# Optimization experiments

Measured on AMD Instinct MI355X. Metric: run time of the kernel, lower is better.

The kernel has to match this reference:

```python
import jax, jax.numpy as jnp
import numpy as np

DIM = 256
HEADS = 4
DIM_HEAD = 32
HIDDEN = HEADS * DIM_HEAD  # 128
SCALE = DIM_HEAD ** -0.5
EPS = 1e-5


def setup_inputs() -> dict:
    key = jax.random.key(0)
    ks = jax.random.split(key, 6)
    b, h, w = 4, 64, 64
    x = jax.random.normal(ks[0], (b, DIM, h, w), dtype=jnp.float32)
    # GroupNorm(1, dim) affine params
    gamma = jnp.ones((DIM,), dtype=jnp.float32)
    beta = jnp.zeros((DIM,), dtype=jnp.float32)
    # 1x1 convs as dense matrices over channels
    w_qkv = jax.random.normal(ks[1], (3 * HIDDEN, DIM), dtype=jnp.float32) * (DIM ** -0.5)
    w_out = jax.random.normal(ks[2], (DIM, HIDDEN), dtype=jnp.float32) * (HIDDEN ** -0.5)
    b_out = jax.random.normal(ks[3], (DIM,), dtype=jnp.float32) * 0.02
    return {"x": x, "gamma": gamma, "beta": beta, "w_qkv": w_qkv,
            "w_out": w_out, "b_out": b_out}


def reference(x, gamma, beta, w_qkv, w_out, b_out):
    b, c, h, w = x.shape
    n = h * w
    # GroupNorm with 1 group == layernorm over (C,H,W) per sample, per-channel affine
    mu = jnp.mean(x, axis=(1, 2, 3), keepdims=True)
    var = jnp.var(x, axis=(1, 2, 3), keepdims=True)
    xn = (x - mu) * jax.lax.rsqrt(var + EPS)
    xn = xn * gamma[None, :, None, None] + beta[None, :, None, None]
    # 1x1 conv -> qkv, then split into heads; flatten spatial dims to n = h*w
    qkv = jnp.einsum('bchw,oc->bohw', xn, w_qkv)            # (b, 3*hidden, h, w)
    qkv = qkv.reshape(b, 3, HEADS, DIM_HEAD, n)
    q, k, v = qkv[:, 0], qkv[:, 1], qkv[:, 2]               # (b, heads, dim_head, n)
    q = q * SCALE
    sim = jnp.einsum('bhci,bhcj->bhij', q, k)               # (b, heads, n, n)
    attn = jax.nn.softmax(sim, axis=-1)                     # stable softmax (max subtract)
    out = jnp.einsum('bhij,bhcj->bhic', attn, v)            # (b, heads, n, dim_head)
    out = out.transpose(0, 1, 3, 2).reshape(b, HIDDEN, h, w)
    y = jnp.einsum('bchw,oc->bohw', out, w_out) + b_out[None, :, None, None]
    return y
```

## Files before the change

kernel.cpp:

```cpp
#include <hip/hip_runtime.h>
#include <math.h>

#define BATCH 4
#define CDIM 256
#define NPIX 4096
#define NPB (CDIM * NPIX)
#define HEADS 4
#define DH 32
#define HID 128
#define OQKV 384
#define QK_SCALE (0.1767766952966369f * 1.44269504088896340736f)
#define SOFTMAX_C 10.0f
#define LN_EPS 1e-5f

typedef _Float16 f16;
typedef _Float16 f16x8 __attribute__((ext_vector_type(8)));
typedef _Float16 f16x4 __attribute__((ext_vector_type(4)));
typedef float f32x4 __attribute__((ext_vector_type(4)));

__device__ __forceinline__ void gload16(const void* g, void* l) {
  __builtin_amdgcn_global_load_lds(
      (const __attribute__((address_space(1))) void*)g,
      (__attribute__((address_space(3))) void*)l, 16, 0, 0);
}

union U8u { unsigned int u[4]; f16x8 v; };
union U8h { f16 h[8]; f16x8 v; };

__global__ __launch_bounds__(256) void ln_reduce(const float* __restrict__ x,
                                                 float* __restrict__ part) {
  const int blk = blockIdx.x;
  const int b = blk >> 6;
  const int slice = blk & 63;
  const float4* xp = (const float4*)(x + (size_t)b * NPB) + (size_t)slice * 4096;
  const int t = threadIdx.x;
  float s = 0.f, ss = 0.f;
#pragma unroll
  for (int k = 0; k < 16; ++k) {
    float4 v = xp[t + k * 256];
    s += v.x + v.y + v.z + v.w;
    ss += v.x * v.x + v.y * v.y + v.z * v.z + v.w * v.w;
  }
#pragma unroll
  for (int d = 1; d < 64; d <<= 1) {
    s += __shfl_xor(s, d);
    ss += __shfl_xor(ss, d);
  }
  __shared__ float red[8];
  const int wv = t >> 6;
  if ((t & 63) == 0) { red[wv * 2] = s; red[wv * 2 + 1] = ss; }
  __syncthreads();
  if (t == 0) {
    part[blk * 2]     = red[0] + red[2] + red[4] + red[6];
    part[blk * 2 + 1] = red[1] + red[3] + red[5] + red[7];
  }
}

__global__ void ln_finalize(const float* __restrict__ part, float* __restrict__ stats) {
  const int t = threadIdx.x;
  const int b = t >> 6, lane = t & 63;
  float s  = part[(b * 64 + lane) * 2];
  float ss = part[(b * 64 + lane) * 2 + 1];
#pragma unroll
  for (int d = 1; d < 64; d <<= 1) {
    s += __shfl_xor(s, d);
    ss += __shfl_xor(ss, d);
  }
  if (lane == 0) {
    float mu = s * (1.f / (float)NPB);
    float var = ss * (1.f / (float)NPB) - mu * mu;
    stats[b * 2] = mu;
    stats[b * 2 + 1] = rsqrtf(var + LN_EPS);
  }
}

__global__ __launch_bounds__(256) void qkv_gemm(const float* __restrict__ x,
                                                const float* __restrict__ gamma,
                                                const float* __restrict__ beta,
                                                const float* __restrict__ wqkv,
                                                const float* __restrict__ stats,
                                                f16* __restrict__ qT,
                                                f16* __restrict__ kT,
                                                f16* __restrict__ vO) {
  const int b = blockIdx.z;
  const int oclass = blockIdx.y;
  const int p0 = blockIdx.x * 128;
  const int t = threadIdx.x;
  const int w = t >> 6, lane = t & 63, low4 = lane & 15, quad = lane >> 4;
  const int ow0 = (w >> 1) * 64, pw0 = (w & 1) * 64;
  const float mu = stats[2 * b], rstd = stats[2 * b + 1];
  const float wscale = (oclass == 0) ? QK_SCALE : 1.f;

  __shared__ f16 Ws[128 * 40];
  __shared__ float Xs[32 * 132];

  const int wo = t >> 1, wh = (t & 1) * 16;
  const int xc = t >> 3, xpq = (t & 7) * 16;
  const float* wg = wqkv + (size_t)(oclass * 128 + wo) * CDIM + wh;
  const float* xg = x + ((size_t)b * CDIM + xc) * NPIX + p0 + xpq;

  f32x4 acc[4][4] = {};
  f32x4 wr[4], xr[4];
  {
    const float ga = gamma[xc] * rstd;
    const float bb = beta[xc] - mu * ga;
#pragma unroll
    for (int j = 0; j < 4; ++j) {
      wr[j] = *(const f32x4*)(wg + j * 4);
      f32x4 r = *(const f32x4*)(xg + j * 4);
      r[0] = r[0] * ga + bb; r[1] = r[1] * ga + bb;
      r[2] = r[2] * ga + bb; r[3] = r[3] * ga + bb;
      xr[j] = r;
    }
  }

  for (int ks = 0; ks < 8; ++ks) {
    __syncthreads();
    {
      U8h h0, h1;
#pragma unroll
      for (int e = 0; e < 4; ++e) {
        h0.h[e]     = (f16)(wr[0][e] * wscale);
        h0.h[4 + e] = (f16)(wr[1][e] * wscale);
        h1.h[e]     = (f16)(wr[2][e] * wscale);
        h1.h[4 + e] = (f16)(wr[3][e] * wscale);
      }
      *(f16x8*)&Ws[wo * 40 + wh]     = h0.v;
      *(f16x8*)&Ws[wo * 40 + wh + 8] = h1.v;
#pragma unroll
      for (int j = 0; j < 4; ++j)
        *(f32x4*)&Xs[xc * 132 + xpq + 4 * j] = xr[j];
    }
    __syncthreads();

    if (ks < 7) {
      const int k0n = (ks + 1) * 32;
      const float ga = gamma[k0n + xc] * rstd;
      const float bb = beta[k0n + xc] - mu * ga;
#pragma unroll
      for (int j = 0; j < 4; ++j) {
        wr[j] = *(const f32x4*)(wg + k0n + j * 4);
        f32x4 r = *(const f32x4*)(xg + (size_t)k0n * NPIX + j * 4);
        r[0] = r[0] * ga + bb; r[1] = r[1] * ga + bb;
        r[2] = r[2] * ga + bb; r[3] = r[3] * ga + bb;
        xr[j] = r;
      }
    }

    f16x8 wf[4], xf[4];
#pragma unroll
    for (int i = 0; i < 4; ++i)
      wf[i] = *(const f16x8*)&Ws[(ow0 + i * 16 + low4) * 40 + quad * 8];
#pragma unroll
    for (int j = 0; j < 4; ++j) {
      const int pl = pw0 + j * 16 + low4;
      U8u xv;
#pragma unroll
      for (int r = 0; r < 4; ++r) {
        const float e0 = Xs[(quad * 8 + 2 * r) * 132 + pl];
        const float e1 = Xs[(quad * 8 + 2 * r + 1) * 132 + pl];
        xv.u[r] = __builtin_bit_cast(unsigned int,
                    __builtin_amdgcn_cvt_pkrtz(e0, e1));
      }
      xf[j] = xv.v;
    }

    if (oclass < 2) {
#pragma unroll
      for (int i = 0; i < 4; ++i)
#pragma unroll
        for (int j = 0; j < 4; ++j)
          acc[i][j] = __builtin_amdgcn_mfma_f32_16x16x32_f16(wf[i], xf[j], acc[i][j], 0, 0, 0);
    } else {
#pragma unroll
      for (int i = 0; i < 4; ++i)
#pragma unroll
        for (int j = 0; j < 4; ++j)
          acc[i][j] = __builtin_amdgcn_mfma_f32_16x16x32_f16(xf[i], wf[j], acc[i][j], 0, 0, 0);
    }
  }

  if (oclass < 2) {
    f16* dst = (oclass == 0) ? qT : kT;
#pragma unroll
    for (int i = 0; i < 4; ++i) {
      const int o_loc = ow0 + i * 16 + quad * 4;
      const int hh = o_loc >> 5;
      const int cb = o_loc & 31;
      f16* base = dst + ((size_t)(b * HEADS + hh) * NPIX) * DH + cb;
#pragma unroll
      for (int j = 0; j < 4; ++j) {
        const int p = p0 + pw0 + j * 16 + low4;
        f16x4 v = {(f16)acc[i][j][0], (f16)acc[i][j][1],
                   (f16)acc[i][j][2], (f16)acc[i][j][3]};
        *(f16x4*)(base + (size_t)p * DH) = v;
      }
    }
  } else {
#pragma unroll
    for (int j = 0; j < 4; ++j) {
      const int o_loc = ow0 + j * 16 + low4;
      const int hh = o_loc >> 5;
      const int cc = o_loc & 31;
      f16* base = vO + ((size_t)(b * HEADS + hh) * DH + cc) * NPIX;
#pragma unroll
      for (int i = 0; i < 4; ++i) {
        const int p = p0 + pw0 + i * 16 + quad * 4;
        f16x4 v = {(f16)acc[i][j][0], (f16)acc[i][j][1],
                   (f16)acc[i][j][2], (f16)acc[i][j][3]};
        *(f16x4*)(base + p) = v;
      }
    }
  }
}

__global__ __launch_bounds__(256) void attn_kernel(const f16* __restrict__ qT,
                                                   const f16* __restrict__ kT,
                                                   const f16* __restrict__ vO,
                                                   f16* __restrict__ obufT) {
  const int bh_idx = blockIdx.x;
  const int i0 = blockIdx.y * 128;
  const int h = bh_idx & 3;
  const int b = bh_idx >> 2;
  const int t = threadIdx.x;
  const int w = t >> 6;
  const int lane = t & 63;
  const int low4 = lane & 15;
  const int quad = lane >> 4;

  __shared__ f16 Ks[2][2048];
  __shared__ f16 Vs[2][2048];

  const size_t bh = (size_t)(b * HEADS + h);
  const f16* kTb = kT + bh * NPIX * DH;
  const f16* vb  = vO + bh * DH * NPIX;

  const int vn = w * 64 + lane;
  const int vc = vn >> 3;
  const int vjc = (vn & 7) ^ (vc & 7);
  const f16* vgbase = vb + (size_t)vc * NPIX + vjc * 8;
  const f16* kgbase = kTb + (size_t)(w * 64 + lane) * 8;

  const f16x8 qf0 = *(const f16x8*)(qT + (bh * NPIX + i0 + w * 32 + low4) * DH + quad * 8);
  const f16x8 qf1 = *(const f16x8*)(qT + (bh * NPIX + i0 + w * 32 + 16 + low4) * DH + quad * 8);

  f32x4 ov00 = {0,0,0,0}, ov01 = {0,0,0,0};
  f32x4 ov10 = {0,0,0,0}, ov11 = {0,0,0,0};
  float lp0 = 0.f, lp1 = 0.f;
  const f32x4 cinit = {-SOFTMAX_C, -SOFTMAX_C, -SOFTMAX_C, -SOFTMAX_C};

  union U4 { unsigned int u[2]; f16x4 v; };

  auto stage = [&](int buf, int jt) {
    gload16(kgbase + (size_t)jt * DH, &Ks[buf][w * 512]);
    gload16(vgbase + jt, &Vs[buf][w * 512]);
  };

  stage(0, 0);
  for (int it = 0; it < NPIX / 64; ++it) {
    const int cur = it & 1;
    __syncthreads();
    if (it + 1 < NPIX / 64) stage(cur ^ 1, (it + 1) * 64);

    f16x8 kf[4];
#pragma unroll
    for (int tt = 0; tt < 4; ++tt)
      kf[tt] = *(const f16x8*)&Ks[cur][(tt * 16 + low4) * 32 + quad * 8];
    f16x4 va[4][2];
#pragma unroll
    for (int tt = 0; tt < 4; ++tt) {
      const int jc16 = tt * 2 + (quad >> 1);
      const int sub = (quad & 1) * 4;
      const int c0 = low4, c1 = low4 + 16;
      va[tt][0] = *(const f16x4*)&Vs[cur][(c0 * 8 + (jc16 ^ (c0 & 7))) * 8 + sub];
      va[tt][1] = *(const f16x4*)&Vs[cur][(c1 * 8 + (jc16 ^ (c1 & 7))) * 8 + sub];
    }

    f32x4 st0[4], st1[4];
#pragma unroll
    for (int tt = 0; tt < 4; ++tt) {
      st0[tt] = __builtin_amdgcn_mfma_f32_16x16x32_f16(kf[tt], qf0, cinit, 0, 0, 0);
      st1[tt] = __builtin_amdgcn_mfma_f32_16x16x32_f16(kf[tt], qf1, cinit, 0, 0, 0);
    }

    U4 pb0[4], pb1[4];
#pragma unroll
    for (int tt = 0; tt < 4; ++tt) {
      const float a0 = __builtin_amdgcn_exp2f(st0[tt][0]);
      const float a1 = __builtin_amdgcn_exp2f(st0[tt][1]);
      const float a2 = __builtin_amdgcn_exp2f(st0[tt][2]);
      const float a3 = __builtin_amdgcn_exp2f(st0[tt][3]);
      lp0 += (a0 + a1) + (a2 + a3);
      pb0[tt].u[0] = __builtin_bit_cast(unsigned int, __builtin_amdgcn_cvt_pkrtz(a0, a1));
      pb0[tt].u[1] = __builtin_bit_cast(unsigned int, __builtin_amdgcn_cvt_pkrtz(a2, a3));
      const float b0 = __builtin_amdgcn_exp2f(st1[tt][0]);
      const float b1 = __builtin_amdgcn_exp2f(st1[tt][1]);
      const float b2 = __builtin_amdgcn_exp2f(st1[tt][2]);
      const float b3 = __builtin_amdgcn_exp2f(st1[tt][3]);
      lp1 += (b0 + b1) + (b2 + b3);
      pb1[tt].u[0] = __builtin_bit_cast(unsigned int, __builtin_amdgcn_cvt_pkrtz(b0, b1));
      pb1[tt].u[1] = __builtin_bit_cast(unsigned int, __builtin_amdgcn_cvt_pkrtz(b2, b3));
    }

#pragma unroll
    for (int tt = 0; tt < 4; ++tt) {
      ov00 = __builtin_amdgcn_mfma_f32_16x16x16f16(va[tt][0], pb0[tt].v, ov00, 0, 0, 0);
      ov01 = __builtin_amdgcn_mfma_f32_16x16x16f16(va[tt][1], pb0[tt].v, ov01, 0, 0, 0);
      ov10 = __builtin_amdgcn_mfma_f32_16x16x16f16(va[tt][0], pb1[tt].v, ov10, 0, 0, 0);
      ov11 = __builtin_amdgcn_mfma_f32_16x16x16f16(va[tt][1], pb1[tt].v, ov11, 0, 0, 0);
    }
  }

  lp0 += __shfl_xor(lp0, 16); lp0 += __shfl_xor(lp0, 32);
  lp1 += __shfl_xor(lp1, 16); lp1 += __shfl_xor(lp1, 32);
  const float inv0 = 1.f / lp0;
  const float inv1 = 1.f / lp1;

  const int pix0 = i0 + w * 32 + low4;
  f16* ob0 = obufT + ((size_t)b * NPIX + pix0) * HID + h * DH + 4 * quad;
  f16* ob1 = ob0 + (size_t)16 * HID;
  {
    f16x4 v00 = {(f16)(ov00[0]*inv0), (f16)(ov00[1]*inv0), (f16)(ov00[2]*inv0), (f16)(ov00[3]*inv0)};
    f16x4 v01 = {(f16)(ov01[0]*inv0), (f16)(ov01[1]*inv0), (f16)(ov01[2]*inv0), (f16)(ov01[3]*inv0)};
    f16x4 v10 = {(f16)(ov10[0]*inv1), (f16)(ov10[1]*inv1), (f16)(ov10[2]*inv1), (f16)(ov10[3]*inv1)};
    f16x4 v11 = {(f16)(ov11[0]*inv1), (f16)(ov11[1]*inv1), (f16)(ov11[2]*inv1), (f16)(ov11[3]*inv1)};
    *(f16x4*)(ob0)      = v00;
    *(f16x4*)(ob0 + 16) = v01;
    *(f16x4*)(ob1)      = v10;
    *(f16x4*)(ob1 + 16) = v11;
  }
}

__global__ __launch_bounds__(256) void out_gemm(const f16* __restrict__ obufT,
                                                const float* __restrict__ wout,
                                                const float* __restrict__ bout,
                                                float* __restrict__ y) {
  const int b = blockIdx.z;
  const int o0 = blockIdx.y * 128;
  const int p0 = blockIdx.x * 128;
  const int t = threadIdx.x;
  const int w = t >> 6, lane = t & 63, low4 = lane & 15, quad = lane >> 4;
  const int ow0 = (w >> 1) * 64, pw0 = (w & 1) * 64;

  __shared__ f16 Ws2[128 * 136];

  {
    const int ro = t >> 1, half = (t & 1) * 64;
    const float* wg = wout + (size_t)(o0 + ro) * HID + half;
#pragma unroll
    for (int jj = 0; jj < 8; ++jj) {
      f32x4 a = *(const f32x4*)(wg + jj * 8);
      f32x4 c = *(const f32x4*)(wg + jj * 8 + 4);
      U8h hv;
      hv.h[0]=(f16)a[0]; hv.h[1]=(f16)a[1]; hv.h[2]=(f16)a[2]; hv.h[3]=(f16)a[3];
      hv.h[4]=(f16)c[0]; hv.h[5]=(f16)c[1]; hv.h[6]=(f16)c[2]; hv.h[7]=(f16)c[3];
      *(f16x8*)&Ws2[ro * 136 + half + jj * 8] = hv.v;
    }
  }
  __syncthreads();

  const f16* bg = obufT + ((size_t)b * NPIX + p0) * HID;

  f32x4 acc[4][4] = {};
#pragma unroll
  for (int ks = 0; ks < 4; ++ks) {
    const int k0 = ks * 32;
    f16x8 af[4], bf[4];
#pragma unroll
    for (int j = 0; j < 4; ++j)
      bf[j] = *(const f16x8*)(bg + (size_t)(pw0 + j * 16 + low4) * HID + k0 + quad * 8);
#pragma unroll
    for (int i = 0; i < 4; ++i)
      af[i] = *(const f16x8*)&Ws2[(ow0 + i * 16 + low4) * 136 + k0 + quad * 8];
#pragma unroll
    for (int i = 0; i < 4; ++i)
#pragma unroll
      for (int j = 0; j < 4; ++j)
        acc[i][j] = __builtin_amdgcn_mfma_f32_16x16x32_f16(af[i], bf[j], acc[i][j], 0, 0, 0);
  }

#pragma unroll
  for (int i = 0; i < 4; ++i) {
    const int ob = o0 + ow0 + i * 16 + quad * 4;
    const float b0v = bout[ob], b1v = bout[ob + 1], b2v = bout[ob + 2], b3v = bout[ob + 3];
    float* yb = y + ((size_t)b * CDIM + ob) * NPIX + p0 + pw0 + low4;
#pragma unroll
    for (int j = 0; j < 4; ++j) {
      yb[j * 16]                       = acc[i][j][0] + b0v;
      yb[(size_t)NPIX + j * 16]       = acc[i][j][1] + b1v;
      yb[(size_t)2 * NPIX + j * 16]   = acc[i][j][2] + b2v;
      yb[(size_t)3 * NPIX + j * 16]   = acc[i][j][3] + b3v;
    }
  }
}

extern "C" void kernel_launch(void* const* d_in, const int* in_sizes, int n_in,
                              void* d_out, int out_size, void* d_ws, size_t ws_size,
                              hipStream_t stream) {
  const float* x     = (const float*)d_in[0];
  const float* gamma = (const float*)d_in[1];
  const float* beta  = (const float*)d_in[2];
  const float* wqkv  = (const float*)d_in[3];
  const float* wout  = (const float*)d_in[4];
  const float* bout  = (const float*)d_in[5];
  float* y = (float*)d_out;

  char* wsb = (char*)d_ws;
  float* part  = (float*)wsb;
  float* stats = part + 512;
  f16* qT = (f16*)(wsb + 4096);
  f16* kT = qT + (size_t)BATCH * HEADS * NPIX * DH;
  f16* vO = kT + (size_t)BATCH * HEADS * NPIX * DH;
  f16* obufT = vO + (size_t)BATCH * HEADS * NPIX * DH;

  ln_reduce<<<dim3(256), 256, 0, stream>>>(x, part);
  ln_finalize<<<dim3(1), 256, 0, stream>>>(part, stats);
  qkv_gemm<<<dim3(32, 3, BATCH), 256, 0, stream>>>(x, gamma, beta, wqkv, stats, qT, kT, vO);
  attn_kernel<<<dim3(16, 32), 256, 0, stream>>>(qT, kT, vO, obufT);
  out_gemm<<<dim3(32, 2, BATCH), 256, 0, stream>>>(obufT, wout, bout, y);
}
```

Before: 168.7 us.

## Split attention block into eight waves with one query tile each and swizzled K

The attention block grows from 4 to 8 waves of 16 query rows each, down from 32 rows, which halves per-wave accumulators and registers and raises the number of resident waves. Staging is split so waves 0-3 load K and waves 4-7 load V. K gets an XOR-swizzled LDS layout to cut bank conflicts on fragment reads. In exchange, each K/V tile loaded into LDS is reused across fewer MFMAs per wave, and the higher wave count adds barrier contention.

Measured after the change: 160.6 us. 4.8% less time.

```diff
diff --git a/kernel.cpp b/kernel.cpp
--- a/kernel.cpp
+++ b/kernel.cpp
@@ -214,10 +214,10 @@
   }
 }
 
-__global__ __launch_bounds__(256) void attn_kernel(const f16* __restrict__ qT,
-                                                   const f16* __restrict__ kT,
-                                                   const f16* __restrict__ vO,
-                                                   f16* __restrict__ obufT) {
+__global__ __launch_bounds__(512, 4) void attn_kernel(const f16* __restrict__ qT,
+                                                      const f16* __restrict__ kT,
+                                                      const f16* __restrict__ vO,
+                                                      f16* __restrict__ obufT) {
   const int bh_idx = blockIdx.x;
   const int i0 = blockIdx.y * 128;
   const int h = bh_idx & 3;
@@ -235,26 +235,28 @@
   const f16* kTb = kT + bh * NPIX * DH;
   const f16* vb  = vO + bh * DH * NPIX;
 
-  const int vn = w * 64 + lane;
+  const int vn = (w & 3) * 64 + lane;
   const int vc = vn >> 3;
   const int vjc = (vn & 7) ^ (vc & 7);
   const f16* vgbase = vb + (size_t)vc * NPIX + vjc * 8;
-  const f16* kgbase = kTb + (size_t)(w * 64 + lane) * 8;
-
-  const f16x8 qf0 = *(const f16x8*)(qT + (bh * NPIX + i0 + w * 32 + low4) * DH + quad * 8);
-  const f16x8 qf1 = *(const f16x8*)(qT + (bh * NPIX + i0 + w * 32 + 16 + low4) * DH + quad * 8);
-
-  f32x4 ov00 = {0,0,0,0}, ov01 = {0,0,0,0};
-  f32x4 ov10 = {0,0,0,0}, ov11 = {0,0,0,0};
-  float lp0 = 0.f, lp1 = 0.f;
+  const int krow = (w & 3) * 16 + (lane >> 2);
+  const int kchk = (lane & 3) ^ ((lane >> 3) & 3);
+  const f16* kgbase = kTb + (size_t)krow * DH + kchk * 8;
+
+  const f16x8 qf = *(const f16x8*)(qT + (bh * NPIX + i0 + w * 16 + low4) * DH + quad * 8);
+
+  f32x4 ov0 = {0, 0, 0, 0}, ov1 = {0, 0, 0, 0};
+  float lp = 0.f;
   const f32x4 cinit = {-SOFTMAX_C, -SOFTMAX_C, -SOFTMAX_C, -SOFTMAX_C};
 
   union U4 { unsigned int u[2]; f16x4 v; };
 
   auto stage = [&](int buf, int jt) {
-    gload16(kgbase + (size_t)jt * DH, &Ks[buf][w * 512]);
-    gload16(vgbase + jt, &Vs[buf][w * 512]);
+    if (w < 4) gload16(kgbase + (size_t)jt * DH, &Ks[buf][(w & 3) * 512]);
+    else       gload16(vgbase + jt,              &Vs[buf][(w & 3) * 512]);
   };
+
+  const int kread_chunk = (quad ^ ((low4 >> 1) & 3)) << 3;
 
   stage(0, 0);
   for (int it = 0; it < NPIX / 64; ++it) {
@@ -265,7 +267,7 @@
     f16x8 kf[4];
 #pragma unroll
     for (int tt = 0; tt < 4; ++tt)
-      kf[tt] = *(const f16x8*)&Ks[cur][(tt * 16 + low4) * 32 + quad * 8];
+      kf[tt] = *(const f16x8*)&Ks[cur][(tt * 16 + low4) * 32 + kread_chunk];
     f16x4 va[4][2];
 #pragma unroll
     for (int tt = 0; tt < 4; ++tt) {
@@ -276,58 +278,41 @@
       va[tt][1] = *(const f16x4*)&Vs[cur][(c1 * 8 + (jc16 ^ (c1 & 7))) * 8 + sub];
     }
 
-    f32x4 st0[4], st1[4];
+    f32x4 st[4];
+#pragma unroll
+    for (int tt = 0; tt < 4; ++tt)
+      st[tt] = __builtin_amdgcn_mfma_f32_16x16x32_f16(kf[tt], qf, cinit, 0, 0, 0);
+
+    U4 pb[4];
 #pragma unroll
     for (int tt = 0; tt < 4; ++tt) {
-      st0[tt] = __builtin_amdgcn_mfma_f32_16x16x32_f16(kf[tt], qf0, cinit, 0, 0, 0);
-      st1[tt] = __builtin_amdgcn_mfma_f32_16x16x32_f16(kf[tt], qf1, cinit, 0, 0, 0);
-    }
-
-    U4 pb0[4], pb1[4];
+      const float a0 = __builtin_amdgcn_exp2f(st[tt][0]);
+      const float a1 = __builtin_amdgcn_exp2f(st[tt][1]);
+      const float a2 = __builtin_amdgcn_exp2f(st[tt][2]);
+      const float a3 = __builtin_amdgcn_exp2f(st[tt][3]);
+      lp += (a0 + a1) + (a2 + a3);
+      pb[tt].u[0] = __builtin_bit_cast(unsigned int, __builtin_amdgcn_cvt_pkrtz(a0, a1));
+      pb[tt].u[1] = __builtin_bit_cast(unsigned int, __builtin_amdgcn_cvt_pkrtz(a2, a3));
+    }
+
 #pragma unroll
     for (int tt = 0; tt < 4; ++tt) {
-      const float a0 = __builtin_amdgcn_exp2f(st0[tt][0]);
-      const float a1 = __builtin_amdgcn_exp2f(st0[tt][1]);
-      const float a2 = __builtin_amdgcn_exp2f(st0[tt][2]);
-      const float a3 = __builtin_amdgcn_exp2f(st0[tt][3]);
-      lp0 += (a0 + a1) + (a2 + a3);
-      pb0[tt].u[0] = __builtin_bit_cast(unsigned int, __builtin_amdgcn_cvt_pkrtz(a0, a1));
-      pb0[tt].u[1] = __builtin_bit_cast(unsigned int, __builtin_amdgcn_cvt_pkrtz(a2, a3));
-      const float b0 = __builtin_amdgcn_exp2f(st1[tt][0]);
-      const float b1 = __builtin_amdgcn_exp2f(st1[tt][1]);
-      const float b2 = __builtin_amdgcn_exp2f(st1[tt][2]);
-      const float b3 = __builtin_amdgcn_exp2f(st1[tt][3]);
-      lp1 += (b0 + b1) + (b2 + b3);
-      pb1[tt].u[0] = __builtin_bit_cast(unsigned int, __builtin_amdgcn_cvt_pkrtz(b0, b1));
-      pb1[tt].u[1] = __builtin_bit_cast(unsigned int, __builtin_amdgcn_cvt_pkrtz(b2, b3));
-    }
-
-#pragma unroll
-    for (int tt = 0; tt < 4; ++tt) {
-      ov00 = __builtin_amdgcn_mfma_f32_16x16x16f16(va[tt][0], pb0[tt].v, ov00, 0, 0, 0);
-      ov01 = __builtin_amdgcn_mfma_f32_16x16x16f16(va[tt][1], pb0[tt].v, ov01, 0, 0, 0);
-      ov10 = __builtin_amdgcn_mfma_f32_16x16x16f16(va[tt][0], pb1[tt].v, ov10, 0, 0, 0);
-      ov11 = __builtin_amdgcn_mfma_f32_16x16x16f16(va[tt][1], pb1[tt].v, ov11, 0, 0, 0);
-    }
-  }
-
-  lp0 += __shfl_xor(lp0, 16); lp0 += __shfl_xor(lp0, 32);
-  lp1 += __shfl_xor(lp1, 16); lp1 += __shfl_xor(lp1, 32);
-  const float inv0 = 1.f / lp0;
-  const float inv1 = 1.f / lp1;
-
-  const int pix0 = i0 + w * 32 + low4;
-  f16* ob0 = obufT + ((size_t)b * NPIX + pix0) * HID + h * DH + 4 * quad;
-  f16* ob1 = ob0 + (size_t)16 * HID;
+      ov0 = __builtin_amdgcn_mfma_f32_16x16x16f16(va[tt][0], pb[tt].v, ov0, 0, 0, 0);
+      ov1 = __builtin_amdgcn_mfma_f32_16x16x16f16(va[tt][1], pb[tt].v, ov1, 0, 0, 0);
+    }
+  }
+
+  lp += __shfl_xor(lp, 16);
+  lp += __shfl_xor(lp, 32);
+  const float inv = 1.f / lp;
+
+  const int pix0 = i0 + w * 16 + low4;
+  f16* ob = obufT + ((size_t)b * NPIX + pix0) * HID + h * DH + 4 * quad;
   {
-    f16x4 v00 = {(f16)(ov00[0]*inv0), (f16)(ov00[1]*inv0), (f16)(ov00[2]*inv0), (f16)(ov00[3]*inv0)};
-    f16x4 v01 = {(f16)(ov01[0]*inv0), (f16)(ov01[1]*inv0), (f16)(ov01[2]*inv0), (f16)(ov01[3]*inv0)};
-    f16x4 v10 = {(f16)(ov10[0]*inv1), (f16)(ov10[1]*inv1), (f16)(ov10[2]*inv1), (f16)(ov10[3]*inv1)};
-    f16x4 v11 = {(f16)(ov11[0]*inv1), (f16)(ov11[1]*inv1), (f16)(ov11[2]*inv1), (f16)(ov11[3]*inv1)};
-    *(f16x4*)(ob0)      = v00;
-    *(f16x4*)(ob0 + 16) = v01;
-    *(f16x4*)(ob1)      = v10;
-    *(f16x4*)(ob1 + 16) = v11;
+    f16x4 v0 = {(f16)(ov0[0] * inv), (f16)(ov0[1] * inv), (f16)(ov0[2] * inv), (f16)(ov0[3] * inv)};
+    f16x4 v1 = {(f16)(ov1[0] * inv), (f16)(ov1[1] * inv), (f16)(ov1[2] * inv), (f16)(ov1[3] * inv)};
+    *(f16x4*)(ob)      = v0;
+    *(f16x4*)(ob + 16) = v1;
   }
 }
 
@@ -416,6 +401,6 @@
   ln_reduce<<<dim3(256), 256, 0, stream>>>(x, part);
   ln_finalize<<<dim3(1), 256, 0, stream>>>(part, stats);
   qkv_gemm<<<dim3(32, 3, BATCH), 256, 0, stream>>>(x, gamma, beta, wqkv, stats, qT, kT, vO);
-  attn_kernel<<<dim3(16, 32), 256, 0, stream>>>(qT, kT, vO, obufT);
+  attn_kernel<<<dim3(16, 32), 512, 0, stream>>>(qT, kT, vO, obufT);
   out_gemm<<<dim3(32, 2, BATCH), 256, 0, stream>>>(obufT, wout, bout, y);
 }
```
